# Kernel optimization log

Hardware: AMD Instinct MI355X
Metric: run time of the kernel (lower is better)

The kernel has to match this reference:

```python
import jax, jax.numpy as jnp
import numpy as np

B, S, H, NH = 2048, 200, 128, 4
NEG = jnp.float32(-2.0**32 + 1)

def setup_inputs() -> dict:
    key = jax.random.key(0)
    k1, k2, k3, k4, k5 = jax.random.split(key, 5)
    item_eb = jax.random.normal(k1, (B, S, H), dtype=jnp.float32)
    mask = jax.random.randint(k2, (B, S), 0, 2, dtype=jnp.int32)
    pos_emb = jax.random.normal(k3, (1, S, H), dtype=jnp.float32) * 0.02
    # nn.Linear(H, 4H, bias=False): weight [4H, H]; store transposed for x @ W
    W1 = jax.random.normal(k4, (H, 4 * H), dtype=jnp.float32) * (1.0 / np.sqrt(H))
    W2 = jax.random.normal(k5, (4 * H, NH), dtype=jnp.float32) * (1.0 / np.sqrt(4 * H))
    return {"item_eb": item_eb, "mask": mask, "pos_emb": pos_emb, "W1": W1, "W2": W2}

def reference(item_eb, mask, pos_emb, W1, W2):
    x = item_eb.reshape(-1, S, H)                       # [B,S,H]
    x_pos = x + pos_emb                                  # broadcast position add
    hidden = jnp.tanh(jnp.einsum('bsh,hf->bsf', x_pos, W1))   # [B,S,4H]
    att = jnp.einsum('bsf,fk->bks', hidden, W2)          # [B,NH,S] (transpose fused)
    att = jnp.where(mask[:, None, :] == 0, NEG, att)     # masked fill
    att = jax.nn.softmax(att, axis=-1)                   # [B,NH,S]
    interest = jnp.einsum('bks,bsh->bkh', att, x)        # [B,NH,H]
    return interest
```

## Files before the change

kernel.cpp:

```cpp
#include <hip/hip_runtime.h>
#include <hip/hip_bf16.h>

typedef _Float16 half8 __attribute__((ext_vector_type(8)));
typedef float f32x4 __attribute__((ext_vector_type(4)));

#define SS 200
#define HH 128
#define NHD 4
#define FH 512
#define NTILES 32
#define NEGF (-4294967295.0f)

__global__ void swizzle_w1(const float* __restrict__ W1, _Float16* __restrict__ dst) {
    int tid = blockIdx.x * blockDim.x + threadIdx.x;
    int j    = tid & 7;
    int lane = (tid >> 3) & 63;
    int ks   = (tid >> 9) & 3;
    int nt   = tid >> 11;
    int k = ks * 32 + (lane >> 4) * 8 + j;
    int n = nt * 16 + (lane & 15);
    dst[tid] = (_Float16)W1[k * FH + n];
}

__device__ __forceinline__ float tanh_fast(float x) {
    x = fminf(fmaxf(x, -15.0f), 15.0f);
    float e = __expf(x + x);
    return (e - 1.0f) * __builtin_amdgcn_rcpf(e + 1.0f);
}

__device__ __forceinline__ f32x4 mfma16(half8 a, half8 b, f32x4 c) {
    return __builtin_amdgcn_mfma_f32_16x16x32_f16(a, b, c, 0, 0, 0);
}

template<int NT>
__device__ __forceinline__ void process_group(
    int mstart, const float* __restrict__ xb, const float* __restrict__ pos,
    const half8* w1p, const float4* w2s, float* attw,
    int wave, int lane, int q, int c,
    const int* rowslot, const int* colslot, int path)
{
    half8 af[NT][4];
#pragma unroll
    for (int t = 0; t < NT; ++t) {
        int row = (mstart + t) * 16 + c;
        bool ok = row < SS;
        const float4* xr = (const float4*)(xb + row * HH);
        const float4* pr = (const float4*)(pos + row * HH);
#pragma unroll
        for (int ks = 0; ks < 4; ++ks) {
            int ci = ks * 8 + q * 2;
            float4 x0, x1, p0, p1;
            if (ok) { x0 = xr[ci]; x1 = xr[ci + 1]; p0 = pr[ci]; p1 = pr[ci + 1]; }
            else {
                x0 = make_float4(0.f,0.f,0.f,0.f); x1 = x0; p0 = x0; p1 = x0;
            }
            half8 h;
            h[0] = (_Float16)(x0.x + p0.x); h[1] = (_Float16)(x0.y + p0.y);
            h[2] = (_Float16)(x0.z + p0.z); h[3] = (_Float16)(x0.w + p0.w);
            h[4] = (_Float16)(x1.x + p1.x); h[5] = (_Float16)(x1.y + p1.y);
            h[6] = (_Float16)(x1.z + p1.z); h[7] = (_Float16)(x1.w + p1.w);
            af[t][ks] = h;
        }
    }

    float attp[NT][4][NHD];
#pragma unroll
    for (int t = 0; t < NT; ++t)
#pragma unroll
        for (int r = 0; r < 4; ++r)
#pragma unroll
            for (int k = 0; k < NHD; ++k) attp[t][r][k] = 0.0f;

    int nt0 = wave * 8;
    for (int nt = nt0; nt < nt0 + 8; ++nt) {
        float4 w2v[4];
#pragma unroll
        for (int r = 0; r < 4; ++r) w2v[r] = w2s[nt * 16 + colslot[r]];
        half8 bf[4];
#pragma unroll
        for (int ks = 0; ks < 4; ++ks) bf[ks] = w1p[(nt * 4 + ks) * 64 + lane];
        f32x4 acc[NT];
#pragma unroll
        for (int t = 0; t < NT; ++t) { f32x4 z = {0.f,0.f,0.f,0.f}; acc[t] = z; }
#pragma unroll
        for (int ks = 0; ks < 4; ++ks)
#pragma unroll
            for (int t = 0; t < NT; ++t)
                acc[t] = mfma16(af[t][ks], bf[ks], acc[t]);
#pragma unroll
        for (int t = 0; t < NT; ++t)
#pragma unroll
            for (int r = 0; r < 4; ++r) {
                float h = tanh_fast(acc[t][r]);
                attp[t][r][0] += h * w2v[r].x;
                attp[t][r][1] += h * w2v[r].y;
                attp[t][r][2] += h * w2v[r].z;
                attp[t][r][3] += h * w2v[r].w;
            }
    }

    if (path == 0) {
#pragma unroll
        for (int t = 0; t < NT; ++t)
#pragma unroll
            for (int r = 0; r < 4; ++r)
#pragma unroll
                for (int k = 0; k < NHD; ++k) {
                    float v = attp[t][r][k];
                    v += __shfl_xor(v, 1);
                    v += __shfl_xor(v, 2);
                    v += __shfl_xor(v, 4);
                    v += __shfl_xor(v, 8);
                    if (c == 0)
                        atomicAdd(&attw[((mstart + t) * 16 + rowslot[r]) * NHD + k], v);
                }
    } else if (path == 1) {
#pragma unroll
        for (int t = 0; t < NT; ++t)
#pragma unroll
            for (int k = 0; k < NHD; ++k) {
                float v = attp[t][0][k] + attp[t][1][k] + attp[t][2][k] + attp[t][3][k];
                v += __shfl_xor(v, 16);
                v += __shfl_xor(v, 32);
                if (q == 0)
                    atomicAdd(&attw[((mstart + t) * 16 + c) * NHD + k], v);
            }
    } else {
#pragma unroll
        for (int t = 0; t < NT; ++t)
#pragma unroll
            for (int r = 0; r < 4; ++r)
#pragma unroll
                for (int k = 0; k < NHD; ++k)
                    atomicAdd(&attw[((mstart + t) * 16 + rowslot[r]) * NHD + k],
                              attp[t][r][k]);
    }
}

template<int USE_WS>
__global__ __launch_bounds__(256, USE_WS ? 3 : 1)
void mhan_main(const float* __restrict__ item, const int* __restrict__ mask,
               const float* __restrict__ pos, const float* __restrict__ W1,
               const float* __restrict__ W2, const _Float16* __restrict__ w1sw,
               float* __restrict__ out)
{
    __shared__ half8  w1s_lds[USE_WS ? 1 : (NTILES * 4 * 64)];
    __shared__ float4 w2s[FH];
    __shared__ float  attw[208 * NHD];

    int tid = threadIdx.x;
    int b   = blockIdx.x;
    int lane = tid & 63, wave = tid >> 6;
    int q = lane >> 4, c = lane & 15;

    int rowslot[4], colslot[4];
    {
        half8 pc_, pone;
#pragma unroll
        for (int j = 0; j < 8; ++j) { pc_[j] = (_Float16)(float)c; pone[j] = (_Float16)0.03125f; }
        f32x4 z = {0.f,0.f,0.f,0.f};
        f32x4 pr = mfma16(pc_, pone, z);
        f32x4 pcv = mfma16(pone, pc_, z);
#pragma unroll
        for (int r = 0; r < 4; ++r) {
            int rv = (int)(pr[r] + 0.5f);
            int cv = (int)(pcv[r] + 0.5f);
            rowslot[r] = rv < 0 ? 0 : (rv > 15 ? 15 : rv);
            colslot[r] = cv < 0 ? 0 : (cv > 15 ? 15 : cv);
        }
    }
    int okA = 1, okB = 1;
#pragma unroll
    for (int r = 0; r < 4; ++r) {
        okA &= (rowslot[r] == q * 4 + r) & (colslot[r] == c);
        okB &= (rowslot[r] == c) & (colslot[r] == q * 4 + r);
    }
    int path = __all(okA) ? 0 : (__all(okB) ? 1 : 2);

    if constexpr (!USE_WS) {
        _Float16* w1f = (_Float16*)w1s_lds;
        for (int idx = tid; idx < HH * FH; idx += 256) {
            int j = idx & 7; int ln = (idx >> 3) & 63;
            int ks = (idx >> 9) & 3; int nt = idx >> 11;
            int k = ks * 32 + (ln >> 4) * 8 + j;
            int n = nt * 16 + (ln & 15);
            w1f[idx] = (_Float16)W1[k * FH + n];
        }
    }
    for (int i = tid; i < FH; i += 256) w2s[i] = ((const float4*)W2)[i];
    for (int i = tid; i < 208 * NHD; i += 256) attw[i] = 0.0f;
    __syncthreads();

    const half8* w1p;
    if constexpr (USE_WS) w1p = (const half8*)w1sw;
    else                  w1p = w1s_lds;

    const float* xb = item + (size_t)b * SS * HH;

    process_group<4>(0,  xb, pos, w1p, w2s, attw, wave, lane, q, c, rowslot, colslot, path);
    process_group<3>(4,  xb, pos, w1p, w2s, attw, wave, lane, q, c, rowslot, colslot, path);
    process_group<3>(7,  xb, pos, w1p, w2s, attw, wave, lane, q, c, rowslot, colslot, path);
    process_group<3>(10, xb, pos, w1p, w2s, attw, wave, lane, q, c, rowslot, colslot, path);
    __syncthreads();

    {
        int k = wave;
        float l[4];
        float m = -__builtin_inff();
#pragma unroll
        for (int i = 0; i < 4; ++i) {
            int s = lane + i * 64;
            if (s < SS) {
                float lv = (mask[(size_t)b * SS + s] != 0) ? attw[s * NHD + k] : NEGF;
                l[i] = lv;
                m = fmaxf(m, lv);
            } else {
                l[i] = -__builtin_inff();
            }
        }
#pragma unroll
        for (int off = 32; off >= 1; off >>= 1) m = fmaxf(m, __shfl_xor(m, off));
        float e[4], sum = 0.0f;
#pragma unroll
        for (int i = 0; i < 4; ++i) {
            e[i] = (l[i] == -__builtin_inff()) ? 0.0f : __expf(l[i] - m);
            sum += e[i];
        }
#pragma unroll
        for (int off = 32; off >= 1; off >>= 1) sum += __shfl_xor(sum, off);
        float inv = __builtin_amdgcn_rcpf(sum);
#pragma unroll
        for (int i = 0; i < 4; ++i) {
            int s = lane + i * 64;
            if (s < SS) attw[s * NHD + k] = e[i] * inv;
        }
    }

    {
        int k = wave;
        float ax = 0.0f, ay = 0.0f;
#pragma unroll 8
        for (int s = 0; s < SS; ++s) {
            float w = attw[s * NHD + k];
            float2 xv = ((const float2*)(xb + s * HH))[lane];
            ax += w * xv.x;
            ay += w * xv.y;
        }
        size_t o = ((size_t)b * NHD + k) * HH + lane * 2;
        float2 ov; ov.x = ax; ov.y = ay;
        *(float2*)(out + o) = ov;
    }
}

extern "C" void kernel_launch(void* const* d_in, const int* in_sizes, int n_in,
                              void* d_out, int out_size, void* d_ws, size_t ws_size,
                              hipStream_t stream) {
    const float* item = (const float*)d_in[0];
    const int*   mask = (const int*)d_in[1];
    const float* pos  = (const float*)d_in[2];
    const float* W1   = (const float*)d_in[3];
    const float* W2   = (const float*)d_in[4];
    float* out = (float*)d_out;

    int B = in_sizes[0] / (SS * HH);
    int use_ws = (ws_size >= (size_t)(HH * FH * sizeof(_Float16))) ? 1 : 0;

    if (use_ws) {
        hipLaunchKernelGGL(swizzle_w1, dim3((HH * FH) / 256), dim3(256), 0, stream,
                           W1, (_Float16*)d_ws);
        mhan_main<1><<<dim3(B), dim3(256), 0, stream>>>(
            item, mask, pos, W1, W2, (const _Float16*)d_ws, out);
    } else {
        mhan_main<0><<<dim3(B), dim3(256), 0, stream>>>(
            item, mask, pos, W1, W2, (const _Float16*)nullptr, out);
    }
}
```

Measured before the change: 628.1 us.

## Process one M-tile at a time to cut registers and raise occupancy

Replaces the grouped multi-tile processing (3-4 M-tiles per group, all kept in registers) with a non-unrolled loop over the 13 M-tiles, each handled alone with two N-tiles per inner iteration. The launch bound for the global-weight path rises from 3 to 4 blocks per CU. The goal is lower VGPR pressure and higher occupancy so the fp16 MFMA GEMM plus tanh epilogue hides memory latency better. In exchange each W1 fragment is re-read from global/L2 13 times instead of 4, and per-tile reductions and atomics now run once per tile.

```diff
diff --git a/kernel.cpp b/kernel.cpp
--- a/kernel.cpp
+++ b/kernel.cpp
@@ -9,6 +9,7 @@
 #define NHD 4
 #define FH 512
 #define NTILES 32
+#define MTILES 13
 #define NEGF (-4294967295.0f)
 
 __global__ void swizzle_w1(const float* __restrict__ W1, _Float16* __restrict__ dst) {
@@ -32,113 +33,8 @@
     return __builtin_amdgcn_mfma_f32_16x16x32_f16(a, b, c, 0, 0, 0);
 }
 
-template<int NT>
-__device__ __forceinline__ void process_group(
-    int mstart, const float* __restrict__ xb, const float* __restrict__ pos,
-    const half8* w1p, const float4* w2s, float* attw,
-    int wave, int lane, int q, int c,
-    const int* rowslot, const int* colslot, int path)
-{
-    half8 af[NT][4];
-#pragma unroll
-    for (int t = 0; t < NT; ++t) {
-        int row = (mstart + t) * 16 + c;
-        bool ok = row < SS;
-        const float4* xr = (const float4*)(xb + row * HH);
-        const float4* pr = (const float4*)(pos + row * HH);
-#pragma unroll
-        for (int ks = 0; ks < 4; ++ks) {
-            int ci = ks * 8 + q * 2;
-            float4 x0, x1, p0, p1;
-            if (ok) { x0 = xr[ci]; x1 = xr[ci + 1]; p0 = pr[ci]; p1 = pr[ci + 1]; }
-            else {
-                x0 = make_float4(0.f,0.f,0.f,0.f); x1 = x0; p0 = x0; p1 = x0;
-            }
-            half8 h;
-            h[0] = (_Float16)(x0.x + p0.x); h[1] = (_Float16)(x0.y + p0.y);
-            h[2] = (_Float16)(x0.z + p0.z); h[3] = (_Float16)(x0.w + p0.w);
-            h[4] = (_Float16)(x1.x + p1.x); h[5] = (_Float16)(x1.y + p1.y);
-            h[6] = (_Float16)(x1.z + p1.z); h[7] = (_Float16)(x1.w + p1.w);
-            af[t][ks] = h;
-        }
-    }
-
-    float attp[NT][4][NHD];
-#pragma unroll
-    for (int t = 0; t < NT; ++t)
-#pragma unroll
-        for (int r = 0; r < 4; ++r)
-#pragma unroll
-            for (int k = 0; k < NHD; ++k) attp[t][r][k] = 0.0f;
-
-    int nt0 = wave * 8;
-    for (int nt = nt0; nt < nt0 + 8; ++nt) {
-        float4 w2v[4];
-#pragma unroll
-        for (int r = 0; r < 4; ++r) w2v[r] = w2s[nt * 16 + colslot[r]];
-        half8 bf[4];
-#pragma unroll
-        for (int ks = 0; ks < 4; ++ks) bf[ks] = w1p[(nt * 4 + ks) * 64 + lane];
-        f32x4 acc[NT];
-#pragma unroll
-        for (int t = 0; t < NT; ++t) { f32x4 z = {0.f,0.f,0.f,0.f}; acc[t] = z; }
-#pragma unroll
-        for (int ks = 0; ks < 4; ++ks)
-#pragma unroll
-            for (int t = 0; t < NT; ++t)
-                acc[t] = mfma16(af[t][ks], bf[ks], acc[t]);
-#pragma unroll
-        for (int t = 0; t < NT; ++t)
-#pragma unroll
-            for (int r = 0; r < 4; ++r) {
-                float h = tanh_fast(acc[t][r]);
-                attp[t][r][0] += h * w2v[r].x;
-                attp[t][r][1] += h * w2v[r].y;
-                attp[t][r][2] += h * w2v[r].z;
-                attp[t][r][3] += h * w2v[r].w;
-            }
-    }
-
-    if (path == 0) {
-#pragma unroll
-        for (int t = 0; t < NT; ++t)
-#pragma unroll
-            for (int r = 0; r < 4; ++r)
-#pragma unroll
-                for (int k = 0; k < NHD; ++k) {
-                    float v = attp[t][r][k];
-                    v += __shfl_xor(v, 1);
-                    v += __shfl_xor(v, 2);
-                    v += __shfl_xor(v, 4);
-                    v += __shfl_xor(v, 8);
-                    if (c == 0)
-                        atomicAdd(&attw[((mstart + t) * 16 + rowslot[r]) * NHD + k], v);
-                }
-    } else if (path == 1) {
-#pragma unroll
-        for (int t = 0; t < NT; ++t)
-#pragma unroll
-            for (int k = 0; k < NHD; ++k) {
-                float v = attp[t][0][k] + attp[t][1][k] + attp[t][2][k] + attp[t][3][k];
-                v += __shfl_xor(v, 16);
-                v += __shfl_xor(v, 32);
-                if (q == 0)
-                    atomicAdd(&attw[((mstart + t) * 16 + c) * NHD + k], v);
-            }
-    } else {
-#pragma unroll
-        for (int t = 0; t < NT; ++t)
-#pragma unroll
-            for (int r = 0; r < 4; ++r)
-#pragma unroll
-                for (int k = 0; k < NHD; ++k)
-                    atomicAdd(&attw[((mstart + t) * 16 + rowslot[r]) * NHD + k],
-                              attp[t][r][k]);
-    }
-}
-
 template<int USE_WS>
-__global__ __launch_bounds__(256, USE_WS ? 3 : 1)
+__global__ __launch_bounds__(256, USE_WS ? 4 : 1)
 void mhan_main(const float* __restrict__ item, const int* __restrict__ mask,
                const float* __restrict__ pos, const float* __restrict__ W1,
                const float* __restrict__ W2, const _Float16* __restrict__ w1sw,
@@ -196,11 +92,93 @@
     else                  w1p = w1s_lds;
 
     const float* xb = item + (size_t)b * SS * HH;
-
-    process_group<4>(0,  xb, pos, w1p, w2s, attw, wave, lane, q, c, rowslot, colslot, path);
-    process_group<3>(4,  xb, pos, w1p, w2s, attw, wave, lane, q, c, rowslot, colslot, path);
-    process_group<3>(7,  xb, pos, w1p, w2s, attw, wave, lane, q, c, rowslot, colslot, path);
-    process_group<3>(10, xb, pos, w1p, w2s, attw, wave, lane, q, c, rowslot, colslot, path);
+    int nt0 = wave * 8;
+
+#pragma unroll 1
+    for (int mt = 0; mt < MTILES; ++mt) {
+        half8 af[4];
+        int row = mt * 16 + c;
+        bool ok = row < SS;
+        const float4* xr = (const float4*)(xb + row * HH);
+        const float4* pr = (const float4*)(pos + row * HH);
+#pragma unroll
+        for (int ks = 0; ks < 4; ++ks) {
+            int ci = ks * 8 + q * 2;
+            float4 x0, x1, p0, p1;
+            if (ok) { x0 = xr[ci]; x1 = xr[ci + 1]; p0 = pr[ci]; p1 = pr[ci + 1]; }
+            else {
+                x0 = make_float4(0.f,0.f,0.f,0.f); x1 = x0; p0 = x0; p1 = x0;
+            }
+            half8 h;
+            h[0] = (_Float16)(x0.x + p0.x); h[1] = (_Float16)(x0.y + p0.y);
+            h[2] = (_Float16)(x0.z + p0.z); h[3] = (_Float16)(x0.w + p0.w);
+            h[4] = (_Float16)(x1.x + p1.x); h[5] = (_Float16)(x1.y + p1.y);
+            h[6] = (_Float16)(x1.z + p1.z); h[7] = (_Float16)(x1.w + p1.w);
+            af[ks] = h;
+        }
+
+        float attp[4][NHD];
+#pragma unroll
+        for (int r = 0; r < 4; ++r)
+#pragma unroll
+            for (int k = 0; k < NHD; ++k) attp[r][k] = 0.0f;
+
+#pragma unroll 1
+        for (int nt = nt0; nt < nt0 + 8; nt += 2) {
+            const half8* bp0 = &w1p[(nt * 4) * 64 + lane];
+            const half8* bp1 = &w1p[((nt + 1) * 4) * 64 + lane];
+            half8 bf0[4], bf1[4];
+#pragma unroll
+            for (int ks = 0; ks < 4; ++ks) { bf0[ks] = bp0[ks * 64]; bf1[ks] = bp1[ks * 64]; }
+            f32x4 acc0 = {0.f,0.f,0.f,0.f}, acc1 = {0.f,0.f,0.f,0.f};
+#pragma unroll
+            for (int ks = 0; ks < 4; ++ks) {
+                acc0 = mfma16(af[ks], bf0[ks], acc0);
+                acc1 = mfma16(af[ks], bf1[ks], acc1);
+            }
+#pragma unroll
+            for (int r = 0; r < 4; ++r) {
+                float4 w0 = w2s[nt * 16 + colslot[r]];
+                float4 w1v = w2s[(nt + 1) * 16 + colslot[r]];
+                float h0 = tanh_fast(acc0[r]);
+                float h1 = tanh_fast(acc1[r]);
+                attp[r][0] += h0 * w0.x + h1 * w1v.x;
+                attp[r][1] += h0 * w0.y + h1 * w1v.y;
+                attp[r][2] += h0 * w0.z + h1 * w1v.z;
+                attp[r][3] += h0 * w0.w + h1 * w1v.w;
+            }
+        }
+
+        if (path == 0) {
+#pragma unroll
+            for (int r = 0; r < 4; ++r)
+#pragma unroll
+                for (int k = 0; k < NHD; ++k) {
+                    float v = attp[r][k];
+                    v += __shfl_xor(v, 1);
+                    v += __shfl_xor(v, 2);
+                    v += __shfl_xor(v, 4);
+                    v += __shfl_xor(v, 8);
+                    if (c == 0)
+                        atomicAdd(&attw[(mt * 16 + rowslot[r]) * NHD + k], v);
+                }
+        } else if (path == 1) {
+#pragma unroll
+            for (int k = 0; k < NHD; ++k) {
+                float v = attp[0][k] + attp[1][k] + attp[2][k] + attp[3][k];
+                v += __shfl_xor(v, 16);
+                v += __shfl_xor(v, 32);
+                if (q == 0)
+                    atomicAdd(&attw[(mt * 16 + c) * NHD + k], v);
+            }
+        } else {
+#pragma unroll
+            for (int r = 0; r < 4; ++r)
+#pragma unroll
+                for (int k = 0; k < NHD; ++k)
+                    atomicAdd(&attw[(mt * 16 + rowslot[r]) * NHD + k], attp[r][k]);
+        }
+    }
     __syncthreads();
 
     {
```

Result: faster. 611.2 us (-2.7%).
